# Kernel tuning notes

Measured on AMD Instinct MI355X. Metric: run time of the kernel, lower is better.

## Reference

```python
import jax, jax.numpy as jnp
import numpy as np

N = 50000   # nodes
C = 64      # channels (in == out)
E = 800000  # edges (before self-loops)
EPS = 1e-5  # BatchNorm eps


def _bn(h, gamma, beta):
    # training-mode BatchNorm1d over the node (batch) axis
    mu = h.mean(0)
    var = h.var(0)
    return (h - mu) * jax.lax.rsqrt(var + EPS) * gamma + beta


def setup_inputs() -> dict:
    key = jax.random.key(0)
    ks = jax.random.split(key, 20)
    p = lambda i, shape, s=0.1: jax.random.normal(ks[i], shape, jnp.float32) * s
    src = jax.random.randint(ks[2], (E,), 0, N, dtype=jnp.int32)
    # guarantee no self-loops (PointTransformerConv removes then re-adds them)
    dst = (src + 1 + jax.random.randint(ks[3], (E,), 0, N - 1, dtype=jnp.int32)) % N
    return dict(
        x=p(0, (N, C), 1.0),
        pos=p(1, (N, 3), 1.0),
        edge_index=jnp.stack([src, dst]),
        Win=p(4, (C, C)), bin_=p(5, (C,)), gin=jnp.ones((C,), jnp.float32), betain=jnp.zeros((C,), jnp.float32),
        Wv=p(6, (C, C)), Wk=p(7, (C, C)), Wq=p(8, (C, C)),
        P1=p(9, (3, C)), pb1=p(10, (C,)), P2=p(11, (C, C)), pb2=p(12, (C,)),
        A1=p(13, (C, C)), ab1=p(14, (C,)), A2=p(15, (C, C)), ab2=p(16, (C,)),
        Wout=p(17, (C, C)), bout=p(18, (C,)), gout=jnp.ones((C,), jnp.float32), betaout=jnp.zeros((C,), jnp.float32),
    )


def reference(x, pos, edge_index, Win, bin_, gin, betain, Wv, Wk, Wq,
              P1, pb1, P2, pb2, A1, ab1, A2, ab2, Wout, bout, gout, betaout):
    silu = jax.nn.silu
    # mlp_in: Linear + BN + SiLU (plain_last=False)
    x = silu(_bn(x @ Win + bin_, gin, betain))

    # PointTransformerConv (add_self_loops=True)
    loop = jnp.arange(N, dtype=edge_index.dtype)
    src = jnp.concatenate([edge_index[0], loop])  # j
    dst = jnp.concatenate([edge_index[1], loop])  # i

    v = x @ Wv       # lin (values), bias=False
    k = x @ Wk       # lin_src
    q = x @ Wq       # lin_dst

    # per-edge positional encoding: pos_nn = SiLU(SiLU((pos_i - pos_j) P1 + b) P2 + b)
    delta = silu(silu((pos[dst] - pos[src]) @ P1 + pb1) @ P2 + pb2)  # [Etot, C]
    # attention logits: attn_nn(alpha_i - alpha_j + delta)
    alpha = q[dst] - k[src] + delta
    alpha = silu(silu(alpha @ A1 + ab1) @ A2 + ab2)

    # segment-wise (per-dst-node, per-channel) softmax over neighborhoods
    m = jax.ops.segment_max(alpha, dst, num_segments=N)
    ex = jnp.exp(alpha - m[dst])
    denom = jax.ops.segment_sum(ex, dst, num_segments=N)
    attn = ex / denom[dst]

    # weighted scatter-reduce of messages
    out = jax.ops.segment_sum(attn * (v[src] + delta), dst, num_segments=N)  # [N, C]

    # mlp_out: Linear + BN, act=None
    return _bn(out @ Wout + bout, gout, betaout)
```

## Files before the change

kernel.cpp:

```cpp
#include <hip/hip_runtime.h>

#define CH 64
#define BN_EPS 1e-5f

typedef __attribute__((ext_vector_type(8))) __bf16 bf16x8;
typedef __attribute__((ext_vector_type(4))) float f32x4;

__device__ __forceinline__ float silu_f(float x) { return x / (1.0f + __expf(-x)); }

__global__ __launch_bounds__(256) void k_lin_in(
    const float* __restrict__ x, const float* __restrict__ Win, const float* __restrict__ bin,
    float* __restrict__ h, float* __restrict__ ssum, float* __restrict__ ssq, int N)
{
    __shared__ float xt[64 * 64];
    __shared__ float Wl[64 * 64];
    __shared__ float red[2][4][64];
    const int t = threadIdx.x, c = t & 63, g = t >> 6;
    const int row0 = blockIdx.x * 64;

    for (int i = t; i < 64 * 64; i += 256) {
        int r = i >> 6, cc = i & 63;
        int gr = row0 + r;
        xt[i] = (gr < N) ? x[(size_t)gr * CH + cc] : 0.0f;
        Wl[i] = Win[i];
    }
    __syncthreads();

    float acc[16];
    const float b = bin[c];
#pragma unroll
    for (int i = 0; i < 16; ++i) acc[i] = b;
    for (int k = 0; k < 64; ++k) {
        float w = Wl[k * 64 + c];
#pragma unroll
        for (int i = 0; i < 16; ++i) acc[i] += xt[(g * 16 + i) * 64 + k] * w;
    }
    float s = 0.0f, ss = 0.0f;
#pragma unroll
    for (int i = 0; i < 16; ++i) {
        int gr = row0 + g * 16 + i;
        if (gr < N) {
            h[(size_t)gr * CH + c] = acc[i];
            s += acc[i];
            ss += acc[i] * acc[i];
        }
    }
    red[0][g][c] = s;
    red[1][g][c] = ss;
    __syncthreads();
    if (g == 0) {
        atomicAdd(&ssum[c], red[0][0][c] + red[0][1][c] + red[0][2][c] + red[0][3][c]);
        atomicAdd(&ssq[c],  red[1][0][c] + red[1][1][c] + red[1][2][c] + red[1][3][c]);
    }
}

__global__ void k_stats(const float* __restrict__ ssum, const float* __restrict__ ssq,
                        const float* __restrict__ gamma, const float* __restrict__ beta,
                        float* __restrict__ scale, float* __restrict__ shift, int N)
{
    int c = threadIdx.x;
    float inv = 1.0f / (float)N;
    float mu = ssum[c] * inv;
    float var = ssq[c] * inv - mu * mu;
    float sc = gamma[c] * rsqrtf(var + BN_EPS);
    scale[c] = sc;
    shift[c] = beta[c] - mu * sc;
}

__global__ __launch_bounds__(256) void k_vkq(
    const float* __restrict__ h, const float* __restrict__ scale, const float* __restrict__ shift,
    const float* __restrict__ Wv, const float* __restrict__ Wk, const float* __restrict__ Wq,
    float* __restrict__ vv, float* __restrict__ kk, float* __restrict__ qq, int N)
{
    __shared__ float xt[64 * 64];
    __shared__ float Wl[2][64 * 64];
    const int t = threadIdx.x, c = t & 63, g = t >> 6;
    const int row0 = blockIdx.x * 64;

    for (int i = t; i < 64 * 64; i += 256) {
        int r = i >> 6, cc = i & 63;
        int gr = row0 + r;
        float hv = (gr < N) ? h[(size_t)gr * CH + cc] : 0.0f;
        xt[i] = silu_f(hv * scale[cc] + shift[cc]);
        Wl[0][i] = Wv[i];
        Wl[1][i] = Wk[i];
    }
    __syncthreads();

    for (int m = 0; m < 2; ++m) {
        float acc[16];
#pragma unroll
        for (int i = 0; i < 16; ++i) acc[i] = 0.0f;
        for (int k = 0; k < 64; ++k) {
            float w = Wl[m][k * 64 + c];
#pragma unroll
            for (int i = 0; i < 16; ++i) acc[i] += xt[(g * 16 + i) * 64 + k] * w;
        }
        float* o = (m == 0) ? vv : kk;
#pragma unroll
        for (int i = 0; i < 16; ++i) {
            int gr = row0 + g * 16 + i;
            if (gr < N) o[(size_t)gr * CH + c] = acc[i];
        }
    }
    __syncthreads();
    for (int i = t; i < 64 * 64; i += 256) Wl[0][i] = Wq[i];
    __syncthreads();
    {
        float acc[16];
#pragma unroll
        for (int i = 0; i < 16; ++i) acc[i] = 0.0f;
        for (int k = 0; k < 64; ++k) {
            float w = Wl[0][k * 64 + c];
#pragma unroll
            for (int i = 0; i < 16; ++i) acc[i] += xt[(g * 16 + i) * 64 + k] * w;
        }
#pragma unroll
        for (int i = 0; i < 16; ++i) {
            int gr = row0 + g * 16 + i;
            if (gr < N) qq[(size_t)gr * CH + c] = acc[i];
        }
    }
}

__global__ __launch_bounds__(256) void k_edge_mfma(
    const int* __restrict__ srcA, const int* __restrict__ dstA,
    const float* __restrict__ pos,
    const float* __restrict__ vv, const float* __restrict__ kk, const float* __restrict__ qq,
    const float* __restrict__ P1, const float* __restrict__ pb1,
    const float* __restrict__ P2, const float* __restrict__ pb2,
    const float* __restrict__ A1, const float* __restrict__ ab1,
    const float* __restrict__ A2, const float* __restrict__ ab2,
    float* __restrict__ num, float* __restrict__ den,
    int E, int Etot, int nChunks)
{
    __shared__ __align__(16) __bf16 Wtab[3][8][64][8];
    __shared__ __align__(16) float tbuf[4][16 * 68];

    const int t = threadIdx.x;
    for (int i = t; i < 3 * 4096; i += 256) {
        int mat = i >> 12, r = i & 4095;
        int j = r & 7, lane = (r >> 3) & 63, ksnt = r >> 9;
        int ks = ksnt & 1, nt = ksnt >> 1;
        int k = ks * 32 + ((lane >> 4) & 3) * 8 + j;
        int n = nt * 16 + (lane & 15);
        const float* W = (mat == 0) ? P2 : ((mat == 1) ? A1 : A2);
        Wtab[mat][ksnt][lane][j] = (__bf16)W[k * 64 + n];
    }
    __syncthreads();

    const int l = t & 63, wid = t >> 6;
    const int lg = l >> 4, lm = l & 15;
    float* buf = tbuf[wid];

    float pb1r[4], pb2r[4], ab1r[4], ab2r[4];
    bf16x8 p1f[4];
#pragma unroll
    for (int nt = 0; nt < 4; ++nt) {
        int co = nt * 16 + lm;
        pb1r[nt] = pb1[co]; pb2r[nt] = pb2[co];
        ab1r[nt] = ab1[co]; ab2r[nt] = ab2[co];
        bf16x8 f;
#pragma unroll
        for (int j = 0; j < 8; ++j)
            f[j] = (__bf16)((lg == 0 && j < 3) ? P1[j * 64 + co] : 0.0f);
        p1f[nt] = f;
    }

    for (int ch = blockIdx.x; ch < nChunks; ch += gridDim.x) {
        const int e0 = ch * 64 + wid * 16;
        const int eA = e0 + lm;
        int sA = 0, dA = 0;
        const bool vAv = (eA < Etot);
        if (vAv) {
            if (eA < E) { sA = srcA[eA]; dA = dstA[eA]; }
            else        { sA = dA = eA - E; }
        }

        float pdx = 0.0f, pdy = 0.0f, pdz = 0.0f;
        if (lg == 0 && vAv) {
            pdx = pos[dA * 3 + 0] - pos[sA * 3 + 0];
            pdy = pos[dA * 3 + 1] - pos[sA * 3 + 1];
            pdz = pos[dA * 3 + 2] - pos[sA * 3 + 2];
        }
        bf16x8 af;
        af[0] = (__bf16)pdx; af[1] = (__bf16)pdy; af[2] = (__bf16)pdz;
        af[3] = af[4] = af[5] = af[6] = af[7] = (__bf16)0.0f;

        f32x4 acc[4];
#pragma unroll
        for (int nt = 0; nt < 4; ++nt) {
            f32x4 a; a[0] = a[1] = a[2] = a[3] = pb1r[nt];
            acc[nt] = __builtin_amdgcn_mfma_f32_16x16x32_bf16(af, p1f[nt], a, 0, 0, 0);
        }
#pragma unroll
        for (int nt = 0; nt < 4; ++nt)
#pragma unroll
            for (int jj = 0; jj < 4; ++jj)
                buf[(lg * 4 + jj) * 68 + nt * 16 + lm] = silu_f(acc[nt][jj]);

        const float* rp = &buf[lm * 68 + lg * 8];
        float4 x0 = *(const float4*)(rp);
        float4 x1 = *(const float4*)(rp + 4);
        float4 x2 = *(const float4*)(rp + 32);
        float4 x3 = *(const float4*)(rp + 36);
        bf16x8 aX0, aX1;
        aX0[0]=(__bf16)x0.x; aX0[1]=(__bf16)x0.y; aX0[2]=(__bf16)x0.z; aX0[3]=(__bf16)x0.w;
        aX0[4]=(__bf16)x1.x; aX0[5]=(__bf16)x1.y; aX0[6]=(__bf16)x1.z; aX0[7]=(__bf16)x1.w;
        aX1[0]=(__bf16)x2.x; aX1[1]=(__bf16)x2.y; aX1[2]=(__bf16)x2.z; aX1[3]=(__bf16)x2.w;
        aX1[4]=(__bf16)x3.x; aX1[5]=(__bf16)x3.y; aX1[6]=(__bf16)x3.z; aX1[7]=(__bf16)x3.w;

#pragma unroll
        for (int nt = 0; nt < 4; ++nt) {
            f32x4 a; a[0] = a[1] = a[2] = a[3] = pb2r[nt];
            bf16x8 b0 = *(const bf16x8*)&Wtab[0][nt * 2 + 0][l][0];
            bf16x8 b1 = *(const bf16x8*)&Wtab[0][nt * 2 + 1][l][0];
            a = __builtin_amdgcn_mfma_f32_16x16x32_bf16(aX0, b0, a, 0, 0, 0);
            a = __builtin_amdgcn_mfma_f32_16x16x32_bf16(aX1, b1, a, 0, 0, 0);
            acc[nt] = a;
        }
        float dlt[4][4];
#pragma unroll
        for (int nt = 0; nt < 4; ++nt)
#pragma unroll
            for (int jj = 0; jj < 4; ++jj) {
                float dv = silu_f(acc[nt][jj]);
                dlt[nt][jj] = dv;
                buf[(lg * 4 + jj) * 68 + nt * 16 + lm] = dv;
            }

        const float* qp = qq + (size_t)dA * 64 + lg * 8;
        const float* kp = kk + (size_t)sA * 64 + lg * 8;
        float4 q0 = *(const float4*)(qp);      float4 q1 = *(const float4*)(qp + 4);
        float4 q2 = *(const float4*)(qp + 32); float4 q3 = *(const float4*)(qp + 36);
        float4 k0 = *(const float4*)(kp);      float4 k1 = *(const float4*)(kp + 4);
        float4 k2 = *(const float4*)(kp + 32); float4 k3 = *(const float4*)(kp + 36);
        float4 d0 = *(const float4*)(rp);
        float4 d1 = *(const float4*)(rp + 4);
        float4 d2 = *(const float4*)(rp + 32);
        float4 d3 = *(const float4*)(rp + 36);

        bf16x8 aA0, aA1;
        aA0[0]=(__bf16)(q0.x-k0.x+d0.x); aA0[1]=(__bf16)(q0.y-k0.y+d0.y);
        aA0[2]=(__bf16)(q0.z-k0.z+d0.z); aA0[3]=(__bf16)(q0.w-k0.w+d0.w);
        aA0[4]=(__bf16)(q1.x-k1.x+d1.x); aA0[5]=(__bf16)(q1.y-k1.y+d1.y);
        aA0[6]=(__bf16)(q1.z-k1.z+d1.z); aA0[7]=(__bf16)(q1.w-k1.w+d1.w);
        aA1[0]=(__bf16)(q2.x-k2.x+d2.x); aA1[1]=(__bf16)(q2.y-k2.y+d2.y);
        aA1[2]=(__bf16)(q2.z-k2.z+d2.z); aA1[3]=(__bf16)(q2.w-k2.w+d2.w);
        aA1[4]=(__bf16)(q3.x-k3.x+d3.x); aA1[5]=(__bf16)(q3.y-k3.y+d3.y);
        aA1[6]=(__bf16)(q3.z-k3.z+d3.z); aA1[7]=(__bf16)(q3.w-k3.w+d3.w);

#pragma unroll
        for (int nt = 0; nt < 4; ++nt) {
            f32x4 a; a[0] = a[1] = a[2] = a[3] = ab1r[nt];
            bf16x8 b0 = *(const bf16x8*)&Wtab[1][nt * 2 + 0][l][0];
            bf16x8 b1 = *(const bf16x8*)&Wtab[1][nt * 2 + 1][l][0];
            a = __builtin_amdgcn_mfma_f32_16x16x32_bf16(aA0, b0, a, 0, 0, 0);
            a = __builtin_amdgcn_mfma_f32_16x16x32_bf16(aA1, b1, a, 0, 0, 0);
            acc[nt] = a;
        }
#pragma unroll
        for (int nt = 0; nt < 4; ++nt)
#pragma unroll
            for (int jj = 0; jj < 4; ++jj)
                buf[(lg * 4 + jj) * 68 + nt * 16 + lm] = silu_f(acc[nt][jj]);

        float4 y0 = *(const float4*)(rp);
        float4 y1 = *(const float4*)(rp + 4);
        float4 y2 = *(const float4*)(rp + 32);
        float4 y3 = *(const float4*)(rp + 36);
        bf16x8 aY0, aY1;
        aY0[0]=(__bf16)y0.x; aY0[1]=(__bf16)y0.y; aY0[2]=(__bf16)y0.z; aY0[3]=(__bf16)y0.w;
        aY0[4]=(__bf16)y1.x; aY0[5]=(__bf16)y1.y; aY0[6]=(__bf16)y1.z; aY0[7]=(__bf16)y1.w;
        aY1[0]=(__bf16)y2.x; aY1[1]=(__bf16)y2.y; aY1[2]=(__bf16)y2.z; aY1[3]=(__bf16)y2.w;
        aY1[4]=(__bf16)y3.x; aY1[5]=(__bf16)y3.y; aY1[6]=(__bf16)y3.z; aY1[7]=(__bf16)y3.w;

#pragma unroll
        for (int nt = 0; nt < 4; ++nt) {
            f32x4 a; a[0] = a[1] = a[2] = a[3] = ab2r[nt];
            bf16x8 b0 = *(const bf16x8*)&Wtab[2][nt * 2 + 0][l][0];
            bf16x8 b1 = *(const bf16x8*)&Wtab[2][nt * 2 + 1][l][0];
            a = __builtin_amdgcn_mfma_f32_16x16x32_bf16(aA0 , b0, a, 0, 0, 0);
            a[0] = a[1] = a[2] = a[3] = ab2r[nt];
            a = __builtin_amdgcn_mfma_f32_16x16x32_bf16(aY0, b0, a, 0, 0, 0);
            a = __builtin_amdgcn_mfma_f32_16x16x32_bf16(aY1, b1, a, 0, 0, 0);
            acc[nt] = a;
        }

        float exv[4][4];
#pragma unroll
        for (int nt = 0; nt < 4; ++nt)
#pragma unroll
            for (int jj = 0; jj < 4; ++jj)
                exv[nt][jj] = __expf(silu_f(acc[nt][jj]));

#pragma unroll
        for (int jj = 0; jj < 4; ++jj) {
            const int er = lg * 4 + jj;
            const int eD = e0 + er;
            const bool vD = (eD < Etot);
            const int sD = __shfl(sA, er);
            const int dD = __shfl(dA, er);
            if (vD) {
                const size_t vb = (size_t)sD * 64 + lm;
                const size_t ob = (size_t)dD * 64 + lm;
#pragma unroll
                for (int nt = 0; nt < 4; ++nt) {
                    float vval = vv[vb + nt * 16];
                    float e = exv[nt][jj];
                    atomicAdd(&den[ob + nt * 16], e);
                    atomicAdd(&num[ob + nt * 16], e * (vval + dlt[nt][jj]));
                }
            }
        }
    }
}

__global__ __launch_bounds__(256) void k_out(
    const float* __restrict__ num, const float* __restrict__ den,
    const float* __restrict__ Wout, const float* __restrict__ bout,
    float* __restrict__ o, float* __restrict__ ssum, float* __restrict__ ssq, int N)
{
    __shared__ float xt[64 * 64];
    __shared__ float Wl[64 * 64];
    __shared__ float red[2][4][64];
    const int t = threadIdx.x, c = t & 63, g = t >> 6;
    const int row0 = blockIdx.x * 64;

    for (int i = t; i < 64 * 64; i += 256) {
        int r = i >> 6, cc = i & 63;
        int gr = row0 + r;
        xt[i] = (gr < N) ? num[(size_t)gr * CH + cc] / den[(size_t)gr * CH + cc] : 0.0f;
        Wl[i] = Wout[i];
    }
    __syncthreads();

    float acc[16];
    const float b = bout[c];
#pragma unroll
    for (int i = 0; i < 16; ++i) acc[i] = b;
    for (int k = 0; k < 64; ++k) {
        float w = Wl[k * 64 + c];
#pragma unroll
        for (int i = 0; i < 16; ++i) acc[i] += xt[(g * 16 + i) * 64 + k] * w;
    }
    float s = 0.0f, ss = 0.0f;
#pragma unroll
    for (int i = 0; i < 16; ++i) {
        int gr = row0 + g * 16 + i;
        if (gr < N) {
            o[(size_t)gr * CH + c] = acc[i];
            s += acc[i];
            ss += acc[i] * acc[i];
        }
    }
    red[0][g][c] = s;
    red[1][g][c] = ss;
    __syncthreads();
    if (g == 0) {
        atomicAdd(&ssum[c], red[0][0][c] + red[0][1][c] + red[0][2][c] + red[0][3][c]);
        atomicAdd(&ssq[c],  red[1][0][c] + red[1][1][c] + red[1][2][c] + red[1][3][c]);
    }
}

__global__ void k_final(const float* __restrict__ o, const float* __restrict__ scale,
                        const float* __restrict__ shift, float* __restrict__ out, int total)
{
    int i = blockIdx.x * blockDim.x + threadIdx.x;
    if (i < total) {
        int c = i & 63;
        out[i] = o[i] * scale[c] + shift[c];
    }
}

extern "C" void kernel_launch(void* const* d_in, const int* in_sizes, int n_in,
                              void* d_out, int out_size, void* d_ws, size_t ws_size,
                              hipStream_t stream)
{
    const float* x      = (const float*)d_in[0];
    const float* pos    = (const float*)d_in[1];
    const int*   ei     = (const int*)d_in[2];
    const float* Win    = (const float*)d_in[3];
    const float* bin    = (const float*)d_in[4];
    const float* gin    = (const float*)d_in[5];
    const float* betain = (const float*)d_in[6];
    const float* Wv     = (const float*)d_in[7];
    const float* Wk     = (const float*)d_in[8];
    const float* Wq     = (const float*)d_in[9];
    const float* P1     = (const float*)d_in[10];
    const float* pb1    = (const float*)d_in[11];
    const float* P2     = (const float*)d_in[12];
    const float* pb2    = (const float*)d_in[13];
    const float* A1     = (const float*)d_in[14];
    const float* ab1    = (const float*)d_in[15];
    const float* A2     = (const float*)d_in[16];
    const float* ab2    = (const float*)d_in[17];
    const float* Wout   = (const float*)d_in[18];
    const float* bout   = (const float*)d_in[19];
    const float* gout   = (const float*)d_in[20];
    const float* betaout= (const float*)d_in[21];

    const int N = in_sizes[0] / CH;
    const int E = in_sizes[2] / 2;
    const int Etot = E + N;
    const int* srcA = ei;
    const int* dstA = ei + E;

    float* ws = (float*)d_ws;
    const size_t NC = (size_t)N * CH;
    float* h   = ws;
    float* vv  = h + NC;
    float* kk  = vv + NC;
    float* qq  = kk + NC;
    float* num = qq + NC;
    float* den = num + NC;
    float* st  = den + NC;

    hipMemsetAsync(num, 0, (2 * NC + 512) * sizeof(float), stream);

    const int nb = (N + 63) / 64;
    k_lin_in<<<nb, 256, 0, stream>>>(x, Win, bin, h, st, st + 64, N);
    k_stats<<<1, 64, 0, stream>>>(st, st + 64, gin, betain, st + 128, st + 192, N);
    k_vkq<<<nb, 256, 0, stream>>>(h, st + 128, st + 192, Wv, Wk, Wq, vv, kk, qq, N);

    const int nChunks = (Etot + 63) / 64;
    const int grid = (nChunks < 2048) ? nChunks : 2048;
    k_edge_mfma<<<grid, 256, 0, stream>>>(srcA, dstA, pos, vv, kk, qq,
                                          P1, pb1, P2, pb2, A1, ab1, A2, ab2,
                                          num, den, E, Etot, nChunks);

    k_out<<<nb, 256, 0, stream>>>(num, den, Wout, bout, h, st + 256, st + 320, N);
    k_stats<<<1, 64, 0, stream>>>(st + 256, st + 320, gout, betaout, st + 384, st + 448, N);
    k_final<<<(int)((NC + 255) / 256), 256, 0, stream>>>(h, st + 384, st + 448,
                                                         (float*)d_out, (int)NC);
}
```

Baseline: 524.7 us.

## Store v/k/q in bf16 and software-pipeline edge gathers across chunks

```diff
diff --git a/kernel.cpp b/kernel.cpp
--- a/kernel.cpp
+++ b/kernel.cpp
@@ -70,7 +70,7 @@
 __global__ __launch_bounds__(256) void k_vkq(
     const float* __restrict__ h, const float* __restrict__ scale, const float* __restrict__ shift,
     const float* __restrict__ Wv, const float* __restrict__ Wk, const float* __restrict__ Wq,
-    float* __restrict__ vv, float* __restrict__ kk, float* __restrict__ qq, int N)
+    __bf16* __restrict__ vv, __bf16* __restrict__ kk, __bf16* __restrict__ qq, int N)
 {
     __shared__ float xt[64 * 64];
     __shared__ float Wl[2][64 * 64];
@@ -96,11 +96,11 @@
 #pragma unroll
             for (int i = 0; i < 16; ++i) acc[i] += xt[(g * 16 + i) * 64 + k] * w;
         }
-        float* o = (m == 0) ? vv : kk;
+        __bf16* o = (m == 0) ? vv : kk;
 #pragma unroll
         for (int i = 0; i < 16; ++i) {
             int gr = row0 + g * 16 + i;
-            if (gr < N) o[(size_t)gr * CH + c] = acc[i];
+            if (gr < N) o[(size_t)gr * CH + c] = (__bf16)acc[i];
         }
     }
     __syncthreads();
@@ -118,7 +118,7 @@
 #pragma unroll
         for (int i = 0; i < 16; ++i) {
             int gr = row0 + g * 16 + i;
-            if (gr < N) qq[(size_t)gr * CH + c] = acc[i];
+            if (gr < N) qq[(size_t)gr * CH + c] = (__bf16)acc[i];
         }
     }
 }
@@ -126,7 +126,7 @@
 __global__ __launch_bounds__(256) void k_edge_mfma(
     const int* __restrict__ srcA, const int* __restrict__ dstA,
     const float* __restrict__ pos,
-    const float* __restrict__ vv, const float* __restrict__ kk, const float* __restrict__ qq,
+    const __bf16* __restrict__ vvb, const __bf16* __restrict__ kkb, const __bf16* __restrict__ qqb,
     const float* __restrict__ P1, const float* __restrict__ pb1,
     const float* __restrict__ P2, const float* __restrict__ pb2,
     const float* __restrict__ A1, const float* __restrict__ ab1,
@@ -135,7 +135,7 @@
     int E, int Etot, int nChunks)
 {
     __shared__ __align__(16) __bf16 Wtab[3][8][64][8];
-    __shared__ __align__(16) float tbuf[4][16 * 68];
+    __shared__ __align__(16) __bf16 tb[4][16][72];
 
     const int t = threadIdx.x;
     for (int i = t; i < 3 * 4096; i += 256) {
@@ -149,9 +149,8 @@
     }
     __syncthreads();
 
-    const int l = t & 63, wid = t >> 6;
-    const int lg = l >> 4, lm = l & 15;
-    float* buf = tbuf[wid];
+    const int l = t & 63, wid = t >> 6, lg = l >> 4, lm = l & 15;
+    __bf16* tbw = &tb[wid][0][0];
 
     float pb1r[4], pb2r[4], ab1r[4], ab2r[4];
     bf16x8 p1f[4];
@@ -167,26 +166,58 @@
         p1f[nt] = f;
     }
 
-    for (int ch = blockIdx.x; ch < nChunks; ch += gridDim.x) {
+    int ch = blockIdx.x;
+    if (ch >= nChunks) return;
+
+    int sC = 0, dC = 0;
+    {
+        int eA = ch * 64 + wid * 16 + lm;
+        if (eA < Etot) { if (eA < E) { sC = srcA[eA]; dC = dstA[eA]; } else { sC = dC = eA - E; } }
+    }
+    float pdl[3];
+    bf16x8 qmk0, qmk1;
+    {
+        const float* ps = pos + (size_t)sC * 3;
+        const float* pd = pos + (size_t)dC * 3;
+        pdl[0] = pd[0] - ps[0]; pdl[1] = pd[1] - ps[1]; pdl[2] = pd[2] - ps[2];
+        const __bf16* qp = qqb + (size_t)dC * 64 + lg * 8;
+        const __bf16* kp = kkb + (size_t)sC * 64 + lg * 8;
+        bf16x8 q0 = *(const bf16x8*)qp, q1 = *(const bf16x8*)(qp + 32);
+        bf16x8 k0 = *(const bf16x8*)kp, k1 = *(const bf16x8*)(kp + 32);
+#pragma unroll
+        for (int j = 0; j < 8; ++j) {
+            qmk0[j] = (__bf16)((float)q0[j] - (float)k0[j]);
+            qmk1[j] = (__bf16)((float)q1[j] - (float)k1[j]);
+        }
+    }
+
+    for (;;) {
         const int e0 = ch * 64 + wid * 16;
-        const int eA = e0 + lm;
-        int sA = 0, dA = 0;
-        const bool vAv = (eA < Etot);
-        if (vAv) {
-            if (eA < E) { sA = srcA[eA]; dA = dstA[eA]; }
-            else        { sA = dA = eA - E; }
-        }
-
-        float pdx = 0.0f, pdy = 0.0f, pdz = 0.0f;
-        if (lg == 0 && vAv) {
-            pdx = pos[dA * 3 + 0] - pos[sA * 3 + 0];
-            pdy = pos[dA * 3 + 1] - pos[sA * 3 + 1];
-            pdz = pos[dA * 3 + 2] - pos[sA * 3 + 2];
-        }
+        const int chn = ch + gridDim.x;
+        const bool hn = chn < nChunks;
+
+        int sN = 0, dN = 0;
+        if (hn) {
+            int eA = chn * 64 + wid * 16 + lm;
+            if (eA < Etot) { if (eA < E) { sN = srcA[eA]; dN = dstA[eA]; } else { sN = dN = eA - E; } }
+        }
+
+        int dD[4];
+        __bf16 vpre[4][4];
+#pragma unroll
+        for (int jj = 0; jj < 4; ++jj) {
+            int sD = __shfl(sC, lg * 4 + jj);
+            dD[jj] = __shfl(dC, lg * 4 + jj);
+            const __bf16* vp = vvb + (size_t)sD * 64 + lm;
+#pragma unroll
+            for (int nt = 0; nt < 4; ++nt) vpre[jj][nt] = vp[nt * 16];
+        }
+
         bf16x8 af;
-        af[0] = (__bf16)pdx; af[1] = (__bf16)pdy; af[2] = (__bf16)pdz;
+        af[0] = (lg == 0) ? (__bf16)pdl[0] : (__bf16)0.0f;
+        af[1] = (lg == 0) ? (__bf16)pdl[1] : (__bf16)0.0f;
+        af[2] = (lg == 0) ? (__bf16)pdl[2] : (__bf16)0.0f;
         af[3] = af[4] = af[5] = af[6] = af[7] = (__bf16)0.0f;
-
         f32x4 acc[4];
 #pragma unroll
         for (int nt = 0; nt < 4; ++nt) {
@@ -197,26 +228,15 @@
         for (int nt = 0; nt < 4; ++nt)
 #pragma unroll
             for (int jj = 0; jj < 4; ++jj)
-                buf[(lg * 4 + jj) * 68 + nt * 16 + lm] = silu_f(acc[nt][jj]);
-
-        const float* rp = &buf[lm * 68 + lg * 8];
-        float4 x0 = *(const float4*)(rp);
-        float4 x1 = *(const float4*)(rp + 4);
-        float4 x2 = *(const float4*)(rp + 32);
-        float4 x3 = *(const float4*)(rp + 36);
-        bf16x8 aX0, aX1;
-        aX0[0]=(__bf16)x0.x; aX0[1]=(__bf16)x0.y; aX0[2]=(__bf16)x0.z; aX0[3]=(__bf16)x0.w;
-        aX0[4]=(__bf16)x1.x; aX0[5]=(__bf16)x1.y; aX0[6]=(__bf16)x1.z; aX0[7]=(__bf16)x1.w;
-        aX1[0]=(__bf16)x2.x; aX1[1]=(__bf16)x2.y; aX1[2]=(__bf16)x2.z; aX1[3]=(__bf16)x2.w;
-        aX1[4]=(__bf16)x3.x; aX1[5]=(__bf16)x3.y; aX1[6]=(__bf16)x3.z; aX1[7]=(__bf16)x3.w;
+                tbw[(lg * 4 + jj) * 72 + nt * 16 + lm] = (__bf16)silu_f(acc[nt][jj]);
+        bf16x8 aX0 = *(const bf16x8*)&tbw[lm * 72 + lg * 8];
+        bf16x8 aX1 = *(const bf16x8*)&tbw[lm * 72 + 32 + lg * 8];
 
 #pragma unroll
         for (int nt = 0; nt < 4; ++nt) {
             f32x4 a; a[0] = a[1] = a[2] = a[3] = pb2r[nt];
-            bf16x8 b0 = *(const bf16x8*)&Wtab[0][nt * 2 + 0][l][0];
-            bf16x8 b1 = *(const bf16x8*)&Wtab[0][nt * 2 + 1][l][0];
-            a = __builtin_amdgcn_mfma_f32_16x16x32_bf16(aX0, b0, a, 0, 0, 0);
-            a = __builtin_amdgcn_mfma_f32_16x16x32_bf16(aX1, b1, a, 0, 0, 0);
+            a = __builtin_amdgcn_mfma_f32_16x16x32_bf16(aX0, *(const bf16x8*)&Wtab[0][nt * 2 + 0][l][0], a, 0, 0, 0);
+            a = __builtin_amdgcn_mfma_f32_16x16x32_bf16(aX1, *(const bf16x8*)&Wtab[0][nt * 2 + 1][l][0], a, 0, 0, 0);
             acc[nt] = a;
         }
         float dlt[4][4];
@@ -226,93 +246,77 @@
             for (int jj = 0; jj < 4; ++jj) {
                 float dv = silu_f(acc[nt][jj]);
                 dlt[nt][jj] = dv;
-                buf[(lg * 4 + jj) * 68 + nt * 16 + lm] = dv;
+                tbw[(lg * 4 + jj) * 72 + nt * 16 + lm] = (__bf16)dv;
             }
 
-        const float* qp = qq + (size_t)dA * 64 + lg * 8;
-        const float* kp = kk + (size_t)sA * 64 + lg * 8;
-        float4 q0 = *(const float4*)(qp);      float4 q1 = *(const float4*)(qp + 4);
-        float4 q2 = *(const float4*)(qp + 32); float4 q3 = *(const float4*)(qp + 36);
-        float4 k0 = *(const float4*)(kp);      float4 k1 = *(const float4*)(kp + 4);
-        float4 k2 = *(const float4*)(kp + 32); float4 k3 = *(const float4*)(kp + 36);
-        float4 d0 = *(const float4*)(rp);
-        float4 d1 = *(const float4*)(rp + 4);
-        float4 d2 = *(const float4*)(rp + 32);
-        float4 d3 = *(const float4*)(rp + 36);
-
+        float pdlN[3];
+        bf16x8 qmkN0, qmkN1;
+        if (hn) {
+            const float* ps = pos + (size_t)sN * 3;
+            const float* pd = pos + (size_t)dN * 3;
+            pdlN[0] = pd[0] - ps[0]; pdlN[1] = pd[1] - ps[1]; pdlN[2] = pd[2] - ps[2];
+            const __bf16* qp = qqb + (size_t)dN * 64 + lg * 8;
+            const __bf16* kp = kkb + (size_t)sN * 64 + lg * 8;
+            bf16x8 q0 = *(const bf16x8*)qp, q1 = *(const bf16x8*)(qp + 32);
+            bf16x8 k0 = *(const bf16x8*)kp, k1 = *(const bf16x8*)(kp + 32);
+#pragma unroll
+            for (int j = 0; j < 8; ++j) {
+                qmkN0[j] = (__bf16)((float)q0[j] - (float)k0[j]);
+                qmkN1[j] = (__bf16)((float)q1[j] - (float)k1[j]);
+            }
+        }
+
+        bf16x8 dA0 = *(const bf16x8*)&tbw[lm * 72 + lg * 8];
+        bf16x8 dA1 = *(const bf16x8*)&tbw[lm * 72 + 32 + lg * 8];
         bf16x8 aA0, aA1;
-        aA0[0]=(__bf16)(q0.x-k0.x+d0.x); aA0[1]=(__bf16)(q0.y-k0.y+d0.y);
-        aA0[2]=(__bf16)(q0.z-k0.z+d0.z); aA0[3]=(__bf16)(q0.w-k0.w+d0.w);
-        aA0[4]=(__bf16)(q1.x-k1.x+d1.x); aA0[5]=(__bf16)(q1.y-k1.y+d1.y);
-        aA0[6]=(__bf16)(q1.z-k1.z+d1.z); aA0[7]=(__bf16)(q1.w-k1.w+d1.w);
-        aA1[0]=(__bf16)(q2.x-k2.x+d2.x); aA1[1]=(__bf16)(q2.y-k2.y+d2.y);
-        aA1[2]=(__bf16)(q2.z-k2.z+d2.z); aA1[3]=(__bf16)(q2.w-k2.w+d2.w);
-        aA1[4]=(__bf16)(q3.x-k3.x+d3.x); aA1[5]=(__bf16)(q3.y-k3.y+d3.y);
-        aA1[6]=(__bf16)(q3.z-k3.z+d3.z); aA1[7]=(__bf16)(q3.w-k3.w+d3.w);
+#pragma unroll
+        for (int j = 0; j < 8; ++j) {
+            aA0[j] = (__bf16)((float)qmk0[j] + (float)dA0[j]);
+            aA1[j] = (__bf16)((float)qmk1[j] + (float)dA1[j]);
+        }
 
 #pragma unroll
         for (int nt = 0; nt < 4; ++nt) {
             f32x4 a; a[0] = a[1] = a[2] = a[3] = ab1r[nt];
-            bf16x8 b0 = *(const bf16x8*)&Wtab[1][nt * 2 + 0][l][0];
-            bf16x8 b1 = *(const bf16x8*)&Wtab[1][nt * 2 + 1][l][0];
-            a = __builtin_amdgcn_mfma_f32_16x16x32_bf16(aA0, b0, a, 0, 0, 0);
-            a = __builtin_amdgcn_mfma_f32_16x16x32_bf16(aA1, b1, a, 0, 0, 0);
+            a = __builtin_amdgcn_mfma_f32_16x16x32_bf16(aA0, *(const bf16x8*)&Wtab[1][nt * 2 + 0][l][0], a, 0, 0, 0);
+            a = __builtin_amdgcn_mfma_f32_16x16x32_bf16(aA1, *(const bf16x8*)&Wtab[1][nt * 2 + 1][l][0], a, 0, 0, 0);
             acc[nt] = a;
         }
 #pragma unroll
         for (int nt = 0; nt < 4; ++nt)
 #pragma unroll
             for (int jj = 0; jj < 4; ++jj)
-                buf[(lg * 4 + jj) * 68 + nt * 16 + lm] = silu_f(acc[nt][jj]);
-
-        float4 y0 = *(const float4*)(rp);
-        float4 y1 = *(const float4*)(rp + 4);
-        float4 y2 = *(const float4*)(rp + 32);
-        float4 y3 = *(const float4*)(rp + 36);
-        bf16x8 aY0, aY1;
-        aY0[0]=(__bf16)y0.x; aY0[1]=(__bf16)y0.y; aY0[2]=(__bf16)y0.z; aY0[3]=(__bf16)y0.w;
-        aY0[4]=(__bf16)y1.x; aY0[5]=(__bf16)y1.y; aY0[6]=(__bf16)y1.z; aY0[7]=(__bf16)y1.w;
-        aY1[0]=(__bf16)y2.x; aY1[1]=(__bf16)y2.y; aY1[2]=(__bf16)y2.z; aY1[3]=(__bf16)y2.w;
-        aY1[4]=(__bf16)y3.x; aY1[5]=(__bf16)y3.y; aY1[6]=(__bf16)y3.z; aY1[7]=(__bf16)y3.w;
+                tbw[(lg * 4 + jj) * 72 + nt * 16 + lm] = (__bf16)silu_f(acc[nt][jj]);
+        bf16x8 aY0 = *(const bf16x8*)&tbw[lm * 72 + lg * 8];
+        bf16x8 aY1 = *(const bf16x8*)&tbw[lm * 72 + 32 + lg * 8];
 
 #pragma unroll
         for (int nt = 0; nt < 4; ++nt) {
             f32x4 a; a[0] = a[1] = a[2] = a[3] = ab2r[nt];
-            bf16x8 b0 = *(const bf16x8*)&Wtab[2][nt * 2 + 0][l][0];
-            bf16x8 b1 = *(const bf16x8*)&Wtab[2][nt * 2 + 1][l][0];
-            a = __builtin_amdgcn_mfma_f32_16x16x32_bf16(aA0 , b0, a, 0, 0, 0);
-            a[0] = a[1] = a[2] = a[3] = ab2r[nt];
-            a = __builtin_amdgcn_mfma_f32_16x16x32_bf16(aY0, b0, a, 0, 0, 0);
-            a = __builtin_amdgcn_mfma_f32_16x16x32_bf16(aY1, b1, a, 0, 0, 0);
+            a = __builtin_amdgcn_mfma_f32_16x16x32_bf16(aY0, *(const bf16x8*)&Wtab[2][nt * 2 + 0][l][0], a, 0, 0, 0);
+            a = __builtin_amdgcn_mfma_f32_16x16x32_bf16(aY1, *(const bf16x8*)&Wtab[2][nt * 2 + 1][l][0], a, 0, 0, 0);
             acc[nt] = a;
         }
 
-        float exv[4][4];
-#pragma unroll
-        for (int nt = 0; nt < 4; ++nt)
-#pragma unroll
-            for (int jj = 0; jj < 4; ++jj)
-                exv[nt][jj] = __expf(silu_f(acc[nt][jj]));
-
 #pragma unroll
         for (int jj = 0; jj < 4; ++jj) {
-            const int er = lg * 4 + jj;
-            const int eD = e0 + er;
-            const bool vD = (eD < Etot);
-            const int sD = __shfl(sA, er);
-            const int dD = __shfl(dA, er);
-            if (vD) {
-                const size_t vb = (size_t)sD * 64 + lm;
-                const size_t ob = (size_t)dD * 64 + lm;
+            const int eD = e0 + lg * 4 + jj;
+            if (eD < Etot) {
+                const size_t ob = (size_t)dD[jj] * 64 + lm;
 #pragma unroll
                 for (int nt = 0; nt < 4; ++nt) {
-                    float vval = vv[vb + nt * 16];
-                    float e = exv[nt][jj];
-                    atomicAdd(&den[ob + nt * 16], e);
-                    atomicAdd(&num[ob + nt * 16], e * (vval + dlt[nt][jj]));
+                    float ex = __expf(silu_f(acc[nt][jj]));
+                    atomicAdd(&den[ob + nt * 16], ex);
+                    atomicAdd(&num[ob + nt * 16], ex * ((float)vpre[jj][nt] + dlt[nt][jj]));
                 }
             }
         }
+
+        if (!hn) break;
+        sC = sN; dC = dN;
+        pdl[0] = pdlN[0]; pdl[1] = pdlN[1]; pdl[2] = pdlN[2];
+        qmk0 = qmkN0; qmk1 = qmkN1;
+        ch = chn;
     }
 }
 
@@ -408,24 +412,24 @@
 
     float* ws = (float*)d_ws;
     const size_t NC = (size_t)N * CH;
-    float* h   = ws;
-    float* vv  = h + NC;
-    float* kk  = vv + NC;
-    float* qq  = kk + NC;
-    float* num = qq + NC;
-    float* den = num + NC;
-    float* st  = den + NC;
+    float* h    = ws;
+    float* num  = h + NC;
+    float* den  = num + NC;
+    float* st   = den + NC;
+    __bf16* vvb = (__bf16*)(st + 512);
+    __bf16* kkb = vvb + NC;
+    __bf16* qqb = kkb + NC;
 
     hipMemsetAsync(num, 0, (2 * NC + 512) * sizeof(float), stream);
 
     const int nb = (N + 63) / 64;
     k_lin_in<<<nb, 256, 0, stream>>>(x, Win, bin, h, st, st + 64, N);
     k_stats<<<1, 64, 0, stream>>>(st, st + 64, gin, betain, st + 128, st + 192, N);
-    k_vkq<<<nb, 256, 0, stream>>>(h, st + 128, st + 192, Wv, Wk, Wq, vv, kk, qq, N);
+    k_vkq<<<nb, 256, 0, stream>>>(h, st + 128, st + 192, Wv, Wk, Wq, vvb, kkb, qqb, N);
 
     const int nChunks = (Etot + 63) / 64;
     const int grid = (nChunks < 2048) ? nChunks : 2048;
-    k_edge_mfma<<<grid, 256, 0, stream>>>(srcA, dstA, pos, vv, kk, qq,
+    k_edge_mfma<<<grid, 256, 0, stream>>>(srcA, dstA, pos, vvb, kkb, qqb,
                                           P1, pb1, P2, pb2, A1, ab1, A2, ab2,
                                           num, den, E, Etot, nChunks);
 
```

Measured after the change: 513.5 us. -2.1%, faster.
